# Performance work log

Measured on AMD Instinct MI355X. Metric: run time of the kernel, lower is better.

## Reference

```python
import jax, jax.numpy as jnp
import numpy as np

B, N, M, D, H = 2, 2048, 2048, 1024, 16
HD = D // H          # head_dim = 64
F = int(D * 4.0)     # mlp hidden = 4096
EPS = 1e-5


def layernorm(x, w, b):
    mu = jnp.mean(x, axis=-1, keepdims=True)
    var = jnp.mean(jnp.square(x - mu), axis=-1, keepdims=True)
    return (x - mu) * jax.lax.rsqrt(var + EPS) * w + b


def setup_inputs() -> dict:
    key = jax.random.key(0)
    ks = jax.random.split(key, 8)
    w = lambda k, shape: jax.random.normal(k, shape, dtype=jnp.float32) * 0.02
    return {
        "query": jax.random.normal(ks[0], (B, N, D), dtype=jnp.float32),
        "context": jax.random.normal(ks[1], (B, M, D), dtype=jnp.float32),
        "qpos": jax.random.randint(ks[2], (B, N), 0, N, dtype=jnp.int32),
        "cpos": jax.random.randint(ks[3], (B, M), 0, M, dtype=jnp.int32),
        "Wq_w": w(ks[4], (D, D)), "Wq_b": jnp.zeros((D,), jnp.float32),
        "Wk_w": w(ks[5], (D, D)), "Wk_b": jnp.zeros((D,), jnp.float32),
        "Wv_w": w(ks[6], (D, D)), "Wv_b": jnp.zeros((D,), jnp.float32),
        "qn_w": jnp.ones((HD,), jnp.float32), "qn_b": jnp.zeros((HD,), jnp.float32),
        "kn_w": jnp.ones((HD,), jnp.float32), "kn_b": jnp.zeros((HD,), jnp.float32),
        "ffn_w": jnp.ones((D,), jnp.float32), "ffn_b": jnp.zeros((D,), jnp.float32),
        "fc1_w": w(ks[7], (D, F)), "fc1_b": jnp.zeros((F,), jnp.float32),
        "fc2_w": w(jax.random.fold_in(key, 99), (F, D)), "fc2_b": jnp.zeros((D,), jnp.float32),
    }


def reference(query, context, qpos, cpos,
              Wq_w, Wq_b, Wk_w, Wk_b, Wv_w, Wv_b,
              qn_w, qn_b, kn_w, kn_b,
              ffn_w, ffn_b, fc1_w, fc1_b, fc2_w, fc2_b):
    # rope=None -> qpos/cpos unused (kept for signature fidelity)
    res = query
    # QKV projections, split heads -> (B,H,T,HD)
    Q = (query @ Wq_w + Wq_b).reshape(B, N, H, HD).transpose(0, 2, 1, 3)
    K = (context @ Wk_w + Wk_b).reshape(B, M, H, HD).transpose(0, 2, 1, 3)
    V = (context @ Wv_w + Wv_b).reshape(B, M, H, HD).transpose(0, 2, 1, 3)
    # per-head LayerNorm on q and k
    Q = layernorm(Q, qn_w, qn_b)
    K = layernorm(K, kn_w, kn_b)
    # attention
    scores = jnp.einsum('bhnd,bhmd->bhnm', Q, K) / jnp.sqrt(jnp.float32(HD))
    attn = jax.nn.softmax(scores, axis=-1)
    out = jnp.einsum('bhnm,bhmd->bhnd', attn, V)
    out = out.transpose(0, 2, 1, 3).reshape(B, N, D)
    out = res + out
    # MLP block with pre-norm
    res2 = out
    h = layernorm(out, ffn_w, ffn_b)
    h = jax.nn.gelu(h @ fc1_w + fc1_b, approximate=False)
    h = h @ fc2_w + fc2_b
    return res2 + h
```

## Files before the change

### kernel.cpp

```cpp
#include <hip/hip_runtime.h>
#include <hip/hip_bf16.h>
#include <math.h>

constexpr int Bb  = 2;
constexpr int Nn  = 2048;
constexpr int Mm  = 2048;
constexpr int Dd  = 1024;
constexpr int Hh  = 16;
constexpr int HD  = 64;
constexpr int Ff  = 4096;
constexpr float EPS = 1e-5f;
constexpr float QSCALE = 0.125f * 1.4426950408889634f;
constexpr float SMAX = 12.0f;

typedef __attribute__((ext_vector_type(8))) short bf16x8;
typedef __attribute__((ext_vector_type(4))) short bf16x4;
typedef __attribute__((ext_vector_type(4))) float f32x4;

__device__ inline unsigned short f2bf(float f) {
    __hip_bfloat16 h = __float2bfloat16(f);
    return *reinterpret_cast<unsigned short*>(&h);
}
__device__ inline unsigned short f2bf_rh(float f) {
    union { float f; unsigned u; } c{f};
    return (unsigned short)((c.u + 0x8000u) >> 16);
}
__device__ inline float bf2f(unsigned short u) {
    union { unsigned u; float f; } c{(unsigned)u << 16};
    return c.f;
}

__device__ inline float gelu_fast(float x) {
    float t = x * x;
    float f = fmaf(-0.10295004f, t, -2.30211782f);
    float e = __builtin_amdgcn_exp2f(x * f);
    return x * __builtin_amdgcn_rcpf(1.0f + e);
}

__device__ inline void async_load16(const void* g, void* l) {
    __builtin_amdgcn_global_load_lds(
        (const __attribute__((address_space(1))) void*)g,
        (__attribute__((address_space(3))) void*)l, 16, 0, 0);
}

__device__ inline bf16x8 ld_b64x2(const unsigned short* p) {
    bf16x4 lo = *(const bf16x4*)p;
    bf16x4 hi = *(const bf16x4*)(p + 4);
    bf16x8 r;
#pragma unroll
    for (int i = 0; i < 4; i++) { r[i] = lo[i]; r[i + 4] = hi[i]; }
    return r;
}

__global__ __launch_bounds__(256) void prep_kernel(
    const float* __restrict__ query, const float* __restrict__ context,
    unsigned short* __restrict__ qa, unsigned short* __restrict__ ca,
    const float* __restrict__ W0, const float* __restrict__ W1,
    const float* __restrict__ W2, const float* __restrict__ W3,
    const float* __restrict__ W4,
    unsigned short* __restrict__ T0, unsigned short* __restrict__ T1,
    unsigned short* __restrict__ T2, unsigned short* __restrict__ T3,
    unsigned short* __restrict__ T4)
{
    __shared__ float tile[32][33];
    int bid = blockIdx.x;
    if (bid < 8192) {
        int i = bid * 256 + threadIdx.x;
        const float* x; unsigned short* y; int k;
        if (i < 1048576) { x = query; y = qa; k = i; }
        else { x = context; y = ca; k = i - 1048576; }
        float4 v = reinterpret_cast<const float4*>(x)[k];
        ushort4 o;
        o.x = f2bf(v.x); o.y = f2bf(v.y); o.z = f2bf(v.z); o.w = f2bf(v.w);
        reinterpret_cast<ushort4*>(y)[k] = o;
        return;
    }
    bid -= 8192;
    const float* W; unsigned short* T; int K, Cn, tid;
    if (bid < 3072) {
        int j = bid >> 10; tid = bid & 1023;
        W = (j == 0) ? W0 : (j == 1) ? W1 : W2;
        T = (j == 0) ? T0 : (j == 1) ? T1 : T2;
        K = Dd; Cn = Dd;
    } else if (bid < 7168) {
        tid = bid - 3072; W = W3; T = T3; K = Dd; Cn = Ff;
    } else {
        tid = bid - 7168; W = W4; T = T4; K = Ff; Cn = Dd;
    }
    int xt = Cn >> 5;
    int bx = tid % xt, by = tid / xt;
    int tx = threadIdx.x & 31, ty = threadIdx.x >> 5;
    int c = bx * 32 + tx;
    int kbase = by * 32;
#pragma unroll
    for (int i = ty; i < 32; i += 8)
        tile[i][tx] = W[(size_t)(kbase + i) * Cn + c];
    __syncthreads();
    int k = kbase + tx;
#pragma unroll
    for (int i = ty; i < 32; i += 8)
        T[(size_t)(bx * 32 + i) * K + k] = f2bf(tile[tx][i]);
}

__global__ __launch_bounds__(256) void qkv_fused_kernel(
    const unsigned short* __restrict__ qa, const unsigned short* __restrict__ ca,
    const unsigned short* __restrict__ Wqt, const unsigned short* __restrict__ Wkt,
    const unsigned short* __restrict__ Wvt,
    const float* __restrict__ bq, const float* __restrict__ bk,
    const float* __restrict__ bv,
    const float* __restrict__ qn_w, const float* __restrict__ qn_b,
    const float* __restrict__ kn_w, const float* __restrict__ kn_b,
    unsigned short* __restrict__ Qbh, unsigned short* __restrict__ Kbh,
    unsigned short* __restrict__ Vt_g)
{
    __shared__ __align__(16) unsigned short As[128 * 32];
    __shared__ __align__(16) unsigned short Bs[128 * 32];

    const int bz = blockIdx.z;
    const unsigned short* A  = (bz == 0) ? qa : ca;
    const unsigned short* Bt = (bz == 0) ? Wqt : (bz == 1) ? Wkt : Wvt;
    const float* bias        = (bz == 0) ? bq  : (bz == 1) ? bk  : bv;
    const int K = Dd;

    const int t    = threadIdx.x;
    const int wave = t >> 6;
    const int lane = t & 63;
    const int r0 = blockIdx.y * 128;
    const int c0 = blockIdx.x * 128;
    const int wm = (wave >> 1) * 64;
    const int wn = (wave & 1) * 64;

    f32x4 acc[4][4];
#pragma unroll
    for (int i = 0; i < 4; i++)
#pragma unroll
        for (int j = 0; j < 4; j++) acc[i][j] = (f32x4)0.0f;

    const int row1 = t >> 2, kc = (t & 3) * 8;
    const size_t arow1 = (size_t)(r0 + row1) * K;
    const size_t arow2 = (size_t)(r0 + row1 + 64) * K;
    const size_t brow1 = (size_t)(c0 + row1) * K;
    const size_t brow2 = (size_t)(c0 + row1 + 64) * K;
    char* AsB1 = (char*)As + wave * 1024;
    char* AsB2 = (char*)As + 4096 + wave * 1024;
    char* BsB1 = (char*)Bs + wave * 1024;
    char* BsB2 = (char*)Bs + 4096 + wave * 1024;

    const int m  = lane & 15;
    const int kq = (lane >> 4) * 8;

    for (int k0 = 0; k0 < K; k0 += 32) {
        async_load16(A + arow1 + k0 + kc, AsB1);
        async_load16(A + arow2 + k0 + kc, AsB2);
        async_load16(Bt + brow1 + k0 + kc, BsB1);
        async_load16(Bt + brow2 + k0 + kc, BsB2);
        __syncthreads();

        bf16x8 af[4], bfr[4];
#pragma unroll
        for (int mi = 0; mi < 4; mi++)
            af[mi] = *(const bf16x8*)&As[(wm + mi * 16 + m) * 32 + kq];
#pragma unroll
        for (int nj = 0; nj < 4; nj++)
            bfr[nj] = *(const bf16x8*)&Bs[(wn + nj * 16 + m) * 32 + kq];
#pragma unroll
        for (int mi = 0; mi < 4; mi++)
#pragma unroll
            for (int nj = 0; nj < 4; nj++)
                acc[mi][nj] = __builtin_amdgcn_mfma_f32_16x16x32_bf16(
                    af[mi], bfr[nj], acc[mi][nj], 0, 0, 0);
        __syncthreads();
    }

    const int rowb = r0 + wm + (lane >> 4) * 4;
    const int colb = c0 + wn + m;
#pragma unroll
    for (int nj = 0; nj < 4; nj++) {
        float bvv = bias[colb + nj * 16];
#pragma unroll
        for (int mi = 0; mi < 4; mi++)
#pragma unroll
            for (int r = 0; r < 4; r++) acc[mi][nj][r] += bvv;
    }

    if (bz < 2) {
        unsigned short* O = (bz == 0) ? Qbh : Kbh;
        const float* lw = (bz == 0) ? qn_w : kn_w;
        const float* lb = (bz == 0) ? qn_b : kn_b;
        const float scale = (bz == 0) ? QSCALE : 1.0f;
        const int hcol = c0 + wn;
        float w4[4], b4[4];
#pragma unroll
        for (int nj = 0; nj < 4; nj++) {
            int d = nj * 16 + m;
            w4[nj] = lw[d]; b4[nj] = lb[d];
        }
#pragma unroll
        for (int mi = 0; mi < 4; mi++) {
#pragma unroll
            for (int r = 0; r < 4; r++) {
                float s = (acc[mi][0][r] + acc[mi][1][r]) +
                          (acc[mi][2][r] + acc[mi][3][r]);
                s += __shfl_xor(s, 1); s += __shfl_xor(s, 2);
                s += __shfl_xor(s, 4); s += __shfl_xor(s, 8);
                float mu = s * (1.0f / 64.0f);
                float v2 = 0.f;
#pragma unroll
                for (int nj = 0; nj < 4; nj++) {
                    float dd = acc[mi][nj][r] - mu; v2 += dd * dd;
                }
                v2 += __shfl_xor(v2, 1); v2 += __shfl_xor(v2, 2);
                v2 += __shfl_xor(v2, 4); v2 += __shfl_xor(v2, 8);
                float rstd = rsqrtf(v2 * (1.0f / 64.0f) + EPS);
                size_t base = (size_t)(rowb + mi * 16 + r) * Dd + hcol;
#pragma unroll
                for (int nj = 0; nj < 4; nj++) {
                    int d = nj * 16 + m;
                    O[base + d] = f2bf(
                        ((acc[mi][nj][r] - mu) * rstd * w4[nj] + b4[nj]) * scale);
                }
            }
        }
    } else {
#pragma unroll
        for (int mi = 0; mi < 4; mi++) {
            int row0 = rowb + mi * 16;
            int bidx = row0 >> 11;
            int mtok = row0 & (Mm - 1);
#pragma unroll
            for (int nj = 0; nj < 4; nj++) {
                int col = colb + nj * 16;
                int h = col >> 6, d = col & 63;
                ushort4 o;
                o.x = f2bf(acc[mi][nj][0]);
                o.y = f2bf(acc[mi][nj][1]);
                o.z = f2bf(acc[mi][nj][2]);
                o.w = f2bf(acc[mi][nj][3]);
                *(ushort4*)(Vt_g + (((size_t)(bidx * Hh + h) * HD + d) << 11) + mtok) = o;
            }
        }
    }
}

template <int EPI, int OUTBF>
__global__ __launch_bounds__(256) void gemm_mfma_bt(
    const unsigned short* __restrict__ A,
    const unsigned short* __restrict__ Bt,
    const float* __restrict__ bias, const float* __restrict__ resid,
    void* __restrict__ Cout, int R, int K, int Cn)
{
    __shared__ __align__(16) unsigned short As[128 * 32];
    __shared__ __align__(16) unsigned short Bs[128 * 32];

    const int t    = threadIdx.x;
    const int wave = t >> 6;
    const int lane = t & 63;
    const int r0 = blockIdx.y * 128;
    const int c0 = blockIdx.x * 128;
    const int wm = (wave >> 1) * 64;
    const int wn = (wave & 1) * 64;

    f32x4 acc[4][4];
#pragma unroll
    for (int i = 0; i < 4; i++)
#pragma unroll
        for (int j = 0; j < 4; j++) acc[i][j] = (f32x4)0.0f;

    const int row1 = t >> 2, kc = (t & 3) * 8;
    const size_t arow1 = (size_t)(r0 + row1) * K;
    const size_t arow2 = (size_t)(r0 + row1 + 64) * K;
    const size_t brow1 = (size_t)(c0 + row1) * K;
    const size_t brow2 = (size_t)(c0 + row1 + 64) * K;
    char* AsB1 = (char*)As + wave * 1024;
    char* AsB2 = (char*)As + 4096 + wave * 1024;
    char* BsB1 = (char*)Bs + wave * 1024;
    char* BsB2 = (char*)Bs + 4096 + wave * 1024;

    const int m  = lane & 15;
    const int kq = (lane >> 4) * 8;

    for (int k0 = 0; k0 < K; k0 += 32) {
        async_load16(A + arow1 + k0 + kc, AsB1);
        async_load16(A + arow2 + k0 + kc, AsB2);
        async_load16(Bt + brow1 + k0 + kc, BsB1);
        async_load16(Bt + brow2 + k0 + kc, BsB2);
        __syncthreads();

        bf16x8 af[4], bfr[4];
#pragma unroll
        for (int mi = 0; mi < 4; mi++)
            af[mi] = *(const bf16x8*)&As[(wm + mi * 16 + m) * 32 + kq];
#pragma unroll
        for (int nj = 0; nj < 4; nj++)
            bfr[nj] = *(const bf16x8*)&Bs[(wn + nj * 16 + m) * 32 + kq];
#pragma unroll
        for (int mi = 0; mi < 4; mi++)
#pragma unroll
            for (int nj = 0; nj < 4; nj++)
                acc[mi][nj] = __builtin_amdgcn_mfma_f32_16x16x32_bf16(
                    af[mi], bfr[nj], acc[mi][nj], 0, 0, 0);
        __syncthreads();
    }

    const int rowb = r0 + wm + (lane >> 4) * 4;
    const int colb = c0 + wn + m;
#pragma unroll
    for (int mi = 0; mi < 4; mi++) {
#pragma unroll
        for (int nj = 0; nj < 4; nj++) {
            int col = colb + nj * 16;
            float bv = bias[col];
#pragma unroll
            for (int r = 0; r < 4; r++) {
                int row = rowb + mi * 16 + r;
                float v = acc[mi][nj][r] + bv;
                if (EPI == 1) v = gelu_fast(v);
                if (resid) v += resid[(size_t)row * Cn + col];
                if (OUTBF)
                    ((unsigned short*)Cout)[(size_t)row * Cn + col] = f2bf(v);
                else
                    ((float*)Cout)[(size_t)row * Cn + col] = v;
            }
        }
    }
}

__global__ __launch_bounds__(256) void gemm_fc2_split(
    const unsigned short* __restrict__ A,
    const unsigned short* __restrict__ Bt,
    unsigned short* __restrict__ Part)
{
    constexpr int Kfull = Ff;
    constexpr int Ksub  = Ff / 4;
    constexpr int Cn    = Dd;
    const int split = blockIdx.z;
    const int koff  = split * Ksub;

    __shared__ __align__(16) unsigned short As[128 * 32];
    __shared__ __align__(16) unsigned short Bs[128 * 32];

    const int t    = threadIdx.x;
    const int wave = t >> 6;
    const int lane = t & 63;
    const int r0 = blockIdx.y * 128;
    const int c0 = blockIdx.x * 128;
    const int wm = (wave >> 1) * 64;
    const int wn = (wave & 1) * 64;

    f32x4 acc[4][4];
#pragma unroll
    for (int i = 0; i < 4; i++)
#pragma unroll
        for (int j = 0; j < 4; j++) acc[i][j] = (f32x4)0.0f;

    const int row1 = t >> 2, kc = (t & 3) * 8;
    const size_t arow1 = (size_t)(r0 + row1) * Kfull + koff;
    const size_t arow2 = (size_t)(r0 + row1 + 64) * Kfull + koff;
    const size_t brow1 = (size_t)(c0 + row1) * Kfull + koff;
    const size_t brow2 = (size_t)(c0 + row1 + 64) * Kfull + koff;
    char* AsB1 = (char*)As + wave * 1024;
    char* AsB2 = (char*)As + 4096 + wave * 1024;
    char* BsB1 = (char*)Bs + wave * 1024;
    char* BsB2 = (char*)Bs + 4096 + wave * 1024;

    const int m  = lane & 15;
    const int kq = (lane >> 4) * 8;

    for (int k0 = 0; k0 < Ksub; k0 += 32) {
        async_load16(A + arow1 + k0 + kc, AsB1);
        async_load16(A + arow2 + k0 + kc, AsB2);
        async_load16(Bt + brow1 + k0 + kc, BsB1);
        async_load16(Bt + brow2 + k0 + kc, BsB2);
        __syncthreads();

        bf16x8 af[4], bfr[4];
#pragma unroll
        for (int mi = 0; mi < 4; mi++)
            af[mi] = *(const bf16x8*)&As[(wm + mi * 16 + m) * 32 + kq];
#pragma unroll
        for (int nj = 0; nj < 4; nj++)
            bfr[nj] = *(const bf16x8*)&Bs[(wn + nj * 16 + m) * 32 + kq];
#pragma unroll
        for (int mi = 0; mi < 4; mi++)
#pragma unroll
            for (int nj = 0; nj < 4; nj++)
                acc[mi][nj] = __builtin_amdgcn_mfma_f32_16x16x32_bf16(
                    af[mi], bfr[nj], acc[mi][nj], 0, 0, 0);
        __syncthreads();
    }

    unsigned short* P = Part + (size_t)split * ((size_t)Bb * Nn * Dd);
    const int rowb = r0 + wm + (lane >> 4) * 4;
    const int colb = c0 + wn + m;
#pragma unroll
    for (int mi = 0; mi < 4; mi++)
#pragma unroll
        for (int nj = 0; nj < 4; nj++) {
            int col = colb + nj * 16;
#pragma unroll
            for (int r = 0; r < 4; r++)
                P[(size_t)(rowb + mi * 16 + r) * Cn + col] = f2bf(acc[mi][nj][r]);
        }
}

__global__ __launch_bounds__(256) void fc2_reduce_kernel(
    const unsigned short* __restrict__ Part, const float* __restrict__ bias,
    const float* __restrict__ attn, float* __restrict__ out)
{
    constexpr size_t NEl = (size_t)Bb * Nn * Dd;
    size_t i4 = (size_t)blockIdx.x * 256 + threadIdx.x;
    size_t i = i4 * 4;
    float4 s = *reinterpret_cast<const float4*>(attn + i);
    float4 bv = *reinterpret_cast<const float4*>(bias + (i & (Dd - 1)));
    s.x += bv.x; s.y += bv.y; s.z += bv.z; s.w += bv.w;
#pragma unroll
    for (int sp = 0; sp < 4; sp++) {
        ushort4 u = *reinterpret_cast<const ushort4*>(Part + sp * NEl + i);
        s.x += bf2f(u.x); s.y += bf2f(u.y); s.z += bf2f(u.z); s.w += bf2f(u.w);
    }
    *reinterpret_cast<float4*>(out + i) = s;
}

__global__ __launch_bounds__(256) void ln_row_bf16_kernel(
    const float* __restrict__ X, const float* __restrict__ w,
    const float* __restrict__ b, unsigned short* __restrict__ Y)
{
    int row = blockIdx.x;
    const float* x = X + (size_t)row * Dd;
    int t = threadIdx.x;
    float v[4];
    float s = 0.f;
#pragma unroll
    for (int i = 0; i < 4; i++) { v[i] = x[t + i * 256]; s += v[i]; }
#pragma unroll
    for (int off = 32; off; off >>= 1) s += __shfl_xor(s, off);
    __shared__ float red[4];
    __shared__ float stats[2];
    if ((t & 63) == 0) red[t >> 6] = s;
    __syncthreads();
    if (t == 0) stats[0] = (red[0] + red[1] + red[2] + red[3]) * (1.0f / Dd);
    __syncthreads();
    float mu = stats[0];
    float s2 = 0.f;
#pragma unroll
    for (int i = 0; i < 4; i++) { float d = v[i] - mu; s2 += d * d; }
#pragma unroll
    for (int off = 32; off; off >>= 1) s2 += __shfl_xor(s2, off);
    __syncthreads();
    if ((t & 63) == 0) red[t >> 6] = s2;
    __syncthreads();
    if (t == 0) stats[1] = (red[0] + red[1] + red[2] + red[3]) * (1.0f / Dd);
    __syncthreads();
    float rstd = rsqrtf(stats[1] + EPS);
    unsigned short* y = Y + (size_t)row * Dd;
#pragma unroll
    for (int i = 0; i < 4; i++) {
        int c = t + i * 256;
        y[c] = f2bf((v[i] - mu) * rstd * w[c] + b[c]);
    }
}

__global__ __launch_bounds__(512) void attention_mfma_kernel(
    const unsigned short* __restrict__ Qb,
    const unsigned short* __restrict__ Kb,
    const unsigned short* __restrict__ Vt_g,
    const float* __restrict__ query,
    float* __restrict__ Out)
{
    const int bid = blockIdx.x;
    const int g  = bid & 31;
    const int qt = bid >> 5;
    const int b  = g >> 4;
    const int h  = g & 15;
    const int q0 = qt * 128;

    __shared__ __align__(16) unsigned short Ks[2 * 64 * 32];
    __shared__ __align__(16) unsigned short Vts[2 * 64 * 32];
    __shared__ __align__(16) unsigned short Ps[8 * 16 * 68];

    const int t    = threadIdx.x;
    const int wave = t >> 6;
    const int lane = t & 63;
    const int m16  = lane & 15;
    const int kg   = lane >> 4;

    bf16x8 qf[2];
    {
        const unsigned short* qp =
            Qb + ((size_t)(b * Nn + q0 + wave * 16 + m16) * Dd + h * HD + kg * 8);
        qf[0] = *(const bf16x8*)qp;
        qf[1] = *(const bf16x8*)(qp + 32);
    }

    f32x4 oacc[4];
    float lrow[4];
#pragma unroll
    for (int i = 0; i < 4; i++) { oacc[i] = (f32x4)0.f; lrow[i] = 0.f; }

    const size_t kbase  = (size_t)(b * Mm) * Dd + h * HD;
    const size_t vtbase = ((size_t)(b * Hh + h) * HD) * Mm;
    unsigned short* psw = Ps + wave * (16 * 68);

    const int u    = t & 255;
    const int pan  = t >> 8;
    const int srow = u >> 2;
    const int schk = (u & 3) * 8;
    char* kdst = (char*)Ks  + pan * 4096 + (wave & 3) * 1024;
    char* vdst = (char*)Vts + pan * 4096 + (wave & 3) * 1024;
    const unsigned short* kp0 = Kb + kbase + (size_t)srow * Dd + schk + pan * 32;
    const unsigned short* vp0 = Vt_g + vtbase + (size_t)srow * Mm + schk + pan * 32;

    for (int m0 = 0; m0 < Mm; m0 += 64) {
        __syncthreads();
        async_load16(kp0 + (size_t)m0 * Dd, kdst);
        async_load16(vp0 + m0, vdst);
        __syncthreads();

        f32x4 s[4];
#pragma unroll
        for (int j = 0; j < 4; j++) {
            bf16x8 b0 = *(const bf16x8*)&Ks[(j * 16 + m16) * 32 + kg * 8];
            bf16x8 b1 = *(const bf16x8*)&Ks[2048 + (j * 16 + m16) * 32 + kg * 8];
            f32x4 a = (f32x4)(-SMAX);
            a = __builtin_amdgcn_mfma_f32_16x16x32_bf16(qf[0], b0, a, 0, 0, 0);
            a = __builtin_amdgcn_mfma_f32_16x16x32_bf16(qf[1], b1, a, 0, 0, 0);
            s[j] = a;
        }

#pragma unroll
        for (int r = 0; r < 4; r++) {
            float p0 = __builtin_amdgcn_exp2f(s[0][r]);
            float p1 = __builtin_amdgcn_exp2f(s[1][r]);
            float p2 = __builtin_amdgcn_exp2f(s[2][r]);
            float p3 = __builtin_amdgcn_exp2f(s[3][r]);
            lrow[r] += (p0 + p1) + (p2 + p3);
            int qrow = kg * 4 + r;
            psw[qrow * 68 +  0 + m16] = f2bf_rh(p0);
            psw[qrow * 68 + 16 + m16] = f2bf_rh(p1);
            psw[qrow * 68 + 32 + m16] = f2bf_rh(p2);
            psw[qrow * 68 + 48 + m16] = f2bf_rh(p3);
        }

        bf16x8 pf0 = ld_b64x2(psw + m16 * 68 + kg * 8);
        bf16x8 pf1 = ld_b64x2(psw + m16 * 68 + 32 + kg * 8);
#pragma unroll
        for (int dj = 0; dj < 4; dj++) {
            bf16x8 v0 = *(const bf16x8*)&Vts[(dj * 16 + m16) * 32 + kg * 8];
            bf16x8 v1 = *(const bf16x8*)&Vts[2048 + (dj * 16 + m16) * 32 + kg * 8];
            oacc[dj] = __builtin_amdgcn_mfma_f32_16x16x32_bf16(pf0, v0, oacc[dj], 0, 0, 0);
            oacc[dj] = __builtin_amdgcn_mfma_f32_16x16x32_bf16(pf1, v1, oacc[dj], 0, 0, 0);
        }
    }

#pragma unroll
    for (int r = 0; r < 4; r++) {
        float l = lrow[r];
        l += __shfl_xor(l, 1);
        l += __shfl_xor(l, 2);
        l += __shfl_xor(l, 4);
        l += __shfl_xor(l, 8);
        float inv = 1.0f / l;
        const size_t rowbase =
            (size_t)(b * Nn + q0 + wave * 16 + kg * 4 + r) * Dd + h * HD;
#pragma unroll
        for (int dj = 0; dj < 4; dj++) {
            size_t idx = rowbase + dj * 16 + m16;
            Out[idx] = query[idx] + oacc[dj][r] * inv;
        }
    }
}

extern "C" void kernel_launch(void* const* d_in, const int* in_sizes, int n_in,
                              void* d_out, int out_size, void* d_ws, size_t ws_size,
                              hipStream_t stream)
{
    const float* query   = (const float*)d_in[0];
    const float* context = (const float*)d_in[1];
    const float* Wq_w = (const float*)d_in[4];
    const float* Wq_b = (const float*)d_in[5];
    const float* Wk_w = (const float*)d_in[6];
    const float* Wk_b = (const float*)d_in[7];
    const float* Wv_w = (const float*)d_in[8];
    const float* Wv_b = (const float*)d_in[9];
    const float* qn_w = (const float*)d_in[10];
    const float* qn_b = (const float*)d_in[11];
    const float* kn_w = (const float*)d_in[12];
    const float* kn_b = (const float*)d_in[13];
    const float* ffn_w = (const float*)d_in[14];
    const float* ffn_b = (const float*)d_in[15];
    const float* fc1_w = (const float*)d_in[16];
    const float* fc1_b = (const float*)d_in[17];
    const float* fc2_w = (const float*)d_in[18];
    const float* fc2_b = (const float*)d_in[19];

    constexpr size_t BND = (size_t)Bb * Nn * Dd;
    constexpr size_t BMD = (size_t)Bb * Mm * Dd;
    constexpr size_t DD  = (size_t)Dd * Dd;
    constexpr size_t DF  = (size_t)Dd * Ff;

    const size_t need = BND * 4 + (2 * BND + 3 * BMD) * 2 + (3 * DD + 2 * DF) * 2
                      + 4 * BND * 2;
    if (ws_size < need) return;

    char* p = (char*)d_ws;
    float* attn = (float*)p;                   p += BND * 4;
    unsigned short* Qbh  = (unsigned short*)p; p += BND * 2;
    unsigned short* Kbh  = (unsigned short*)p; p += BMD * 2;
    unsigned short* Vt_g = (unsigned short*)p; p += BMD * 2;
    unsigned short* qa   = (unsigned short*)p; p += BND * 2;
    unsigned short* ca   = (unsigned short*)p; p += BMD * 2;
    unsigned short* Wqt  = (unsigned short*)p; p += DD * 2;
    unsigned short* Wkt  = (unsigned short*)p; p += DD * 2;
    unsigned short* Wvt  = (unsigned short*)p; p += DD * 2;
    unsigned short* fc1t = (unsigned short*)p; p += DF * 2;
    unsigned short* fc2t = (unsigned short*)p; p += DF * 2;
    unsigned short* part = (unsigned short*)p; p += 4 * BND * 2;
    unsigned short* normed = Qbh;
    unsigned short* mid    = Kbh;
    float* out = (float*)d_out;

    const int R = Bb * Nn;
    dim3 blk(256);

    prep_kernel<<<19456, blk, 0, stream>>>(
        query, context, qa, ca,
        Wq_w, Wk_w, Wv_w, fc1_w, fc2_w, Wqt, Wkt, Wvt, fc1t, fc2t);

    qkv_fused_kernel<<<dim3(Dd / 128, R / 128, 3), blk, 0, stream>>>(
        qa, ca, Wqt, Wkt, Wvt, Wq_b, Wk_b, Wv_b,
        qn_w, qn_b, kn_w, kn_b, Qbh, Kbh, Vt_g);

    attention_mfma_kernel<<<Bb * Hh * (Nn / 128), 512, 0, stream>>>(
        Qbh, Kbh, Vt_g, query, attn);

    ln_row_bf16_kernel<<<Bb * Nn, blk, 0, stream>>>(attn, ffn_w, ffn_b, normed);

    gemm_mfma_bt<1, 1><<<dim3(Ff / 128, R / 128), blk, 0, stream>>>(
        normed, fc1t, fc1_b, nullptr, mid, R, Dd, Ff);
    gemm_fc2_split<<<dim3(Dd / 128, R / 128, 4), blk, 0, stream>>>(
        mid, fc2t, part);
    fc2_reduce_kernel<<<BND / 4 / 256, blk, 0, stream>>>(
        part, fc2_b, attn, out);
}
```

Measured before the change: 381.7 us.

## Double-buffer K/V LDS tiles and XOR-swizzle chunks in attention kernel

The attention kernel now keeps two LDS buffers each for the K and V tiles. While the current tile is being consumed, it prefetches the next tile with the async global-to-LDS loads, which removes one __syncthreads per iteration and hides global load latency behind MFMA work. It also XOR-swizzles the 16-byte chunk position by row, on the global-load source side and on the LDS read side, to reduce bank conflicts on the bf16x8 reads. In exchange it doubles K/V LDS usage, and it relies on async_load16 completing before the next top-of-loop barrier.

```diff
diff --git a/kernel.cpp b/kernel.cpp
--- a/kernel.cpp
+++ b/kernel.cpp
@@ -474,8 +474,8 @@
     const int h  = g & 15;
     const int q0 = qt * 128;
 
-    __shared__ __align__(16) unsigned short Ks[2 * 64 * 32];
-    __shared__ __align__(16) unsigned short Vts[2 * 64 * 32];
+    __shared__ __align__(16) unsigned short Ks[2][2 * 64 * 32];
+    __shared__ __align__(16) unsigned short Vts[2][2 * 64 * 32];
     __shared__ __align__(16) unsigned short Ps[8 * 16 * 68];
 
     const int t    = threadIdx.x;
@@ -483,6 +483,7 @@
     const int lane = t & 63;
     const int m16  = lane & 15;
     const int kg   = lane >> 4;
+    const int swc  = (kg ^ ((m16 >> 1) & 3)) << 3;
 
     bf16x8 qf[2];
     {
@@ -504,23 +505,32 @@
     const int u    = t & 255;
     const int pan  = t >> 8;
     const int srow = u >> 2;
-    const int schk = (u & 3) * 8;
-    char* kdst = (char*)Ks  + pan * 4096 + (wave & 3) * 1024;
-    char* vdst = (char*)Vts + pan * 4096 + (wave & 3) * 1024;
+    const int schk = ((u & 3) ^ ((srow >> 1) & 3)) * 8;
+    char* kdstA = (char*)&Ks[0][0]  + pan * 4096 + (wave & 3) * 1024;
+    char* kdstB = (char*)&Ks[1][0]  + pan * 4096 + (wave & 3) * 1024;
+    char* vdstA = (char*)&Vts[0][0] + pan * 4096 + (wave & 3) * 1024;
+    char* vdstB = (char*)&Vts[1][0] + pan * 4096 + (wave & 3) * 1024;
     const unsigned short* kp0 = Kb + kbase + (size_t)srow * Dd + schk + pan * 32;
     const unsigned short* vp0 = Vt_g + vtbase + (size_t)srow * Mm + schk + pan * 32;
 
+    async_load16(kp0, kdstA);
+    async_load16(vp0, vdstA);
+
     for (int m0 = 0; m0 < Mm; m0 += 64) {
         __syncthreads();
-        async_load16(kp0 + (size_t)m0 * Dd, kdst);
-        async_load16(vp0 + m0, vdst);
-        __syncthreads();
+        const int cur = (m0 >> 6) & 1;
+        if (m0 + 64 < Mm) {
+            async_load16(kp0 + (size_t)(m0 + 64) * Dd, cur ? kdstA : kdstB);
+            async_load16(vp0 + (m0 + 64),              cur ? vdstA : vdstB);
+        }
+        const unsigned short* Kc = &Ks[cur][0];
+        const unsigned short* Vc = &Vts[cur][0];
 
         f32x4 s[4];
 #pragma unroll
         for (int j = 0; j < 4; j++) {
-            bf16x8 b0 = *(const bf16x8*)&Ks[(j * 16 + m16) * 32 + kg * 8];
-            bf16x8 b1 = *(const bf16x8*)&Ks[2048 + (j * 16 + m16) * 32 + kg * 8];
+            bf16x8 b0 = *(const bf16x8*)&Kc[(j * 16 + m16) * 32 + swc];
+            bf16x8 b1 = *(const bf16x8*)&Kc[2048 + (j * 16 + m16) * 32 + swc];
             f32x4 a = (f32x4)(-SMAX);
             a = __builtin_amdgcn_mfma_f32_16x16x32_bf16(qf[0], b0, a, 0, 0, 0);
             a = __builtin_amdgcn_mfma_f32_16x16x32_bf16(qf[1], b1, a, 0, 0, 0);
@@ -545,8 +555,8 @@
         bf16x8 pf1 = ld_b64x2(psw + m16 * 68 + 32 + kg * 8);
 #pragma unroll
         for (int dj = 0; dj < 4; dj++) {
-            bf16x8 v0 = *(const bf16x8*)&Vts[(dj * 16 + m16) * 32 + kg * 8];
-            bf16x8 v1 = *(const bf16x8*)&Vts[2048 + (dj * 16 + m16) * 32 + kg * 8];
+            bf16x8 v0 = *(const bf16x8*)&Vc[(dj * 16 + m16) * 32 + swc];
+            bf16x8 v1 = *(const bf16x8*)&Vc[2048 + (dj * 16 + m16) * 32 + swc];
             oacc[dj] = __builtin_amdgcn_mfma_f32_16x16x32_bf16(pf0, v0, oacc[dj], 0, 0, 0);
             oacc[dj] = __builtin_amdgcn_mfma_f32_16x16x32_bf16(pf1, v1, oacc[dj], 0, 0, 0);
         }
```

After: 377.0 us. No clear change (-1.2%).
